# Optimization experiments

Hardware: AMD Instinct MI355X
Metric: run time of the kernel (lower is better)

## Reference

```python
import jax, jax.numpy as jnp
import numpy as np

NUM_HEADS = 16
EPS = 1e-12  # F.normalize default eps


def _l2norm(x):
    # F.normalize(x, dim=-1): x / max(||x||_2, eps)
    n = jnp.sqrt(jnp.sum(x * x, axis=-1, keepdims=True))
    return x / jnp.maximum(n, EPS)


def setup_inputs() -> dict:
    key = jax.random.key(0)
    k1, k2, k3 = jax.random.split(key, 3)
    B, N, C = 16, 3136, 768
    x = jax.random.normal(k1, (B, N, C), dtype=jnp.float32)
    qkv_w = jax.random.normal(k2, (C, 3 * C), dtype=jnp.float32) * (1.0 / np.sqrt(C))
    temperature = jnp.ones((NUM_HEADS, 1, 1), dtype=jnp.float32)
    proj_w = jax.random.normal(k3, (C, C), dtype=jnp.float32) * (1.0 / np.sqrt(C))
    proj_b = jnp.zeros((C,), dtype=jnp.float32)
    return {"x": x, "qkv_w": qkv_w, "temperature": temperature,
            "proj_w": proj_w, "proj_b": proj_b}


def reference(x, qkv_w, temperature, proj_w, proj_b):
    B, N, C = x.shape
    H = NUM_HEADS
    D = C // H
    # qkv: [B,N,3C] -> [B,N,3,H,D] -> (3,B,H,D,N)
    qkv = (x @ qkv_w).reshape(B, N, 3, H, D).transpose(2, 0, 3, 4, 1)
    q, k, v = qkv[0], qkv[1], qkv[2]  # each [B,H,D,N]
    qn = _l2norm(q)  # normalize over token axis N
    kn = _l2norm(k)
    # cross-covariance: [B,H,D,D]
    attn = jnp.einsum('bhdn,bhen->bhde', qn, kn) * temperature
    attn = jax.nn.softmax(attn, axis=-1)
    out = jnp.einsum('bhde,bhen->bhdn', attn, v)  # [B,H,D,N]
    out = out.transpose(0, 3, 1, 2).reshape(B, N, C)
    return out @ proj_w + proj_b
```

## Files before the change

### kernel.cpp

```cpp
#include <hip/hip_runtime.h>

typedef unsigned short u16;
typedef unsigned int   u32;
typedef __attribute__((ext_vector_type(4))) float f32x4;
typedef __attribute__((ext_vector_type(8))) short bf16x8;
typedef __attribute__((ext_vector_type(8))) unsigned short u16x8;

#define MFMA16(a,b,c) __builtin_amdgcn_mfma_f32_16x16x32_bf16(a,b,c,0,0,0)

#define PANEL 2408448u

__device__ __forceinline__ u16 f32_bf16(float f){
  u32 u = __builtin_bit_cast(u32, f);
  u = (u + 0x7FFFu + ((u >> 16) & 1u)) >> 16;
  return (u16)u;
}

__device__ __forceinline__ void async_cp16(const u16* g, u16* l){
  __builtin_amdgcn_global_load_lds((const __attribute__((address_space(1))) u32*)g,
                                   (__attribute__((address_space(3))) u32*)l, 16, 0, 0);
}

__global__ __launch_bounds__(256)
void cvt_f32_bf16(const float* __restrict__ in, u16* __restrict__ out){
  size_t i = ((size_t)blockIdx.x * 256 + threadIdx.x) * 8;
  f32x4 a = *(const f32x4*)(in + i);
  f32x4 b = *(const f32x4*)(in + i + 4);
  u16x8 o;
  o[0]=f32_bf16(a[0]); o[1]=f32_bf16(a[1]); o[2]=f32_bf16(a[2]); o[3]=f32_bf16(a[3]);
  o[4]=f32_bf16(b[0]); o[5]=f32_bf16(b[1]); o[6]=f32_bf16(b[2]); o[7]=f32_bf16(b[3]);
  *(u16x8*)(out + i) = o;
}

__global__ __launch_bounds__(256)
void transpose_cvt(const float* __restrict__ w, u16* __restrict__ wt, int K, int N){
  __shared__ float tile[32][33];
  int n0 = blockIdx.x * 32, k0 = blockIdx.y * 32;
  int tx = threadIdx.x, ty = threadIdx.y;
#pragma unroll
  for (int j = 0; j < 32; j += 8) tile[ty + j][tx] = w[(size_t)(k0 + ty + j) * N + n0 + tx];
  __syncthreads();
#pragma unroll
  for (int j = 0; j < 32; j += 8)
    wt[(size_t)(n0 + ty + j) * K + k0 + tx] = f32_bf16(tile[tx][ty + j]);
}

template<int OUT_BF16, int BIAS, int A_GATHER, int C_HEADS>
__global__ __launch_bounds__(256)
void gemm_bt(const u16* __restrict__ A, const u16* __restrict__ Bt,
             void* __restrict__ Cv, const float* __restrict__ bias,
             int K, int lda, int ldc){
  __shared__ u16 sA[128 * 64];
  __shared__ u16 sB[128 * 64];
  const int tid  = threadIdx.x;
  const int lane = tid & 63;
  const int wave = tid >> 6;
  const int lrow = lane & 15, quad = lane >> 4;
  const int m0 = blockIdx.y * 128, n0 = blockIdx.x * 128;
  const int wm = (wave & 1) * 64, wn = (wave >> 1) * 64;
  const int sw = lrow & 7;
  const int col0 = ((0 * 4 + quad) ^ sw) * 8;
  const int col1 = ((1 * 4 + quad) ^ sw) * 8;

  f32x4 acc[4][4];
#pragma unroll
  for (int i = 0; i < 4; i++)
#pragma unroll
    for (int j = 0; j < 4; j++) acc[i][j] = (f32x4){0.f, 0.f, 0.f, 0.f};

  for (int kt = 0; kt < K; kt += 64){
#pragma unroll
    for (int i = 0; i < 4; i++){
      int c = i * 256 + tid;
      int m = c >> 3, kc = (c & 7) ^ (m & 7);
      const u16* src;
      if (A_GATHER){
        unsigned k0 = (unsigned)(kt + kc * 8);
        unsigned hh = k0 / 48u;
        unsigned dd = k0 - hh * 48u;
        src = A + (size_t)hh * PANEL + (size_t)(m0 + m) * 48 + dd;
      } else {
        src = A + (size_t)(m0 + m) * lda + kt + kc * 8;
      }
      async_cp16(src, &sA[c * 8]);
    }
#pragma unroll
    for (int i = 0; i < 4; i++){
      int c = i * 256 + tid;
      int n = c >> 3, kc = (c & 7) ^ (n & 7);
      async_cp16(Bt + (size_t)(n0 + n) * K + kt + kc * 8, &sB[c * 8]);
    }
    __syncthreads();
#pragma unroll
    for (int kk = 0; kk < 2; kk++){
      const int col = kk ? col1 : col0;
      bf16x8 af[4], bfv[4];
#pragma unroll
      for (int mi = 0; mi < 4; mi++)
        af[mi] = *(const bf16x8*)&sA[(wm + mi * 16 + lrow) * 64 + col];
#pragma unroll
      for (int ni = 0; ni < 4; ni++)
        bfv[ni] = *(const bf16x8*)&sB[(wn + ni * 16 + lrow) * 64 + col];
#pragma unroll
      for (int mi = 0; mi < 4; mi++)
#pragma unroll
        for (int ni = 0; ni < 4; ni++)
          acc[mi][ni] = MFMA16(af[mi], bfv[ni], acc[mi][ni]);
    }
    __syncthreads();
  }
#pragma unroll
  for (int mi = 0; mi < 4; mi++){
#pragma unroll
    for (int ni = 0; ni < 4; ni++){
      int col = n0 + wn + ni * 16 + lrow;
      if (OUT_BF16 && C_HEADS){
        unsigned which = (unsigned)col / 768u;
        unsigned rem   = (unsigned)col - which * 768u;
        unsigned hh    = rem / 48u;
        unsigned dd    = rem - hh * 48u;
        u16* cb = (u16*)Cv + (size_t)(which * 16u + hh) * PANEL + dd;
#pragma unroll
        for (int r = 0; r < 4; r++){
          int row = m0 + wm + mi * 16 + quad * 4 + r;
          cb[(size_t)row * 48] = f32_bf16(acc[mi][ni][r]);
        }
      } else {
        float bv = BIAS ? bias[col] : 0.f;
#pragma unroll
        for (int r = 0; r < 4; r++){
          int row = m0 + wm + mi * 16 + quad * 4 + r;
          float v = acc[mi][ni][r];
          if (OUT_BF16) ((u16*)Cv)[(size_t)row * ldc + col] = f32_bf16(v);
          else          ((float*)Cv)[(size_t)row * ldc + col] = v + bv;
        }
      }
    }
  }
}

__global__ __launch_bounds__(256)
void attn_stats(const u16* __restrict__ qkv2, const float* __restrict__ temperature,
                u16* __restrict__ attnb){
  const int h = blockIdx.x, b = blockIdx.y;
  const int tid = threadIdx.x, wave = tid >> 6, lane = tid & 63;
  const int lrow = lane & 15, quad = lane >> 4;
  __shared__ struct {
    union {
      struct { u16 q[48 * 136]; u16 k[48 * 136]; } t;
      float red[2 * 15 * 256];
    } u;
    float S[48 * 49];
    float invq[48], invk[48];
  } sm;

  f32x4 acc[15];
#pragma unroll
  for (int t = 0; t < 15; t++) acc[t] = (f32x4){0.f, 0.f, 0.f, 0.f};

  const u16* qbase = qkv2 + (size_t)h        * PANEL + (size_t)b * 3136 * 48;
  const u16* kbase = qkv2 + (size_t)(16 + h) * PANEL + (size_t)b * 3136 * 48;

  for (int n0 = 0; n0 < 3136; n0 += 128){
    __syncthreads();
#pragma unroll
    for (int i = 0; i < 3; i++){
      int wgrp = i * 4 + wave;
      int qk = wgrp >= 6;
      int dg = qk ? wgrp - 6 : wgrp;
      int n  = n0 + lane * 2;
      const u16* src = (qk ? kbase : qbase) + (size_t)n * 48 + dg * 8;
      u16x8 va = (n     < 3136) ? *(const u16x8*)src        : (u16x8){0,0,0,0,0,0,0,0};
      u16x8 vb = (n + 1 < 3136) ? *(const u16x8*)(src + 48) : (u16x8){0,0,0,0,0,0,0,0};
      u16* dst = qk ? sm.u.t.k : sm.u.t.q;
#pragma unroll
      for (int j = 0; j < 8; j++)
        *(u32*)&dst[(dg * 8 + j) * 136 + lane * 2] = (u32)va[j] | ((u32)vb[j] << 16);
    }
    __syncthreads();
    bf16x8 qf[3], kf[3];
#pragma unroll
    for (int ti = 0; ti < 3; ti++){
      qf[ti] = *(const bf16x8*)&sm.u.t.q[(ti * 16 + lrow) * 136 + wave * 32 + quad * 8];
      kf[ti] = *(const bf16x8*)&sm.u.t.k[(ti * 16 + lrow) * 136 + wave * 32 + quad * 8];
    }
#pragma unroll
    for (int ti = 0; ti < 3; ti++)
#pragma unroll
      for (int tj = 0; tj < 3; tj++)
        acc[ti * 3 + tj] = MFMA16(qf[ti], kf[tj], acc[ti * 3 + tj]);
#pragma unroll
    for (int ti = 0; ti < 3; ti++){
      acc[9  + ti] = MFMA16(qf[ti], qf[ti], acc[9  + ti]);
      acc[12 + ti] = MFMA16(kf[ti], kf[ti], acc[12 + ti]);
    }
  }
  __syncthreads();
  if (wave < 2){
#pragma unroll
    for (int t = 0; t < 15; t++)
      *(f32x4*)&sm.u.red[(wave * 15 + t) * 256 + lane * 4] = acc[t];
  }
  __syncthreads();
  if (wave >= 2){
#pragma unroll
    for (int t = 0; t < 15; t++){
      f32x4* p = (f32x4*)&sm.u.red[((wave - 2) * 15 + t) * 256 + lane * 4];
      *p = *p + acc[t];
    }
  }
  __syncthreads();
  {
    const int p = tid;
    const int lr = p >> 2, rr = p & 3;
    const int row16 = ((lr >> 4) << 2) + rr, col16 = lr & 15;
#pragma unroll
    for (int t = 0; t < 9; t++){
      float v = sm.u.red[t * 256 + p] + sm.u.red[(15 + t) * 256 + p];
      sm.S[((t / 3) * 16 + row16) * 49 + (t % 3) * 16 + col16] = v;
    }
#pragma unroll
    for (int t = 9; t < 15; t++){
      float v = sm.u.red[t * 256 + p] + sm.u.red[(15 + t) * 256 + p];
      if (row16 == col16){
        if (t < 12) sm.invq[(t - 9)  * 16 + row16] = v;
        else        sm.invk[(t - 12) * 16 + row16] = v;
      }
    }
  }
  __syncthreads();
  if (tid < 96){
    float* arr = (tid < 48) ? sm.invq : sm.invk;
    int d = (tid < 48) ? tid : tid - 48;
    arr[d] = 1.0f / fmaxf(sqrtf(arr[d]), 1e-12f);
  }
  __syncthreads();
  if (tid < 48){
    const int d = tid;
    const float scale = sm.invq[d] * temperature[h];
    float lg[48];
    float mx = -1e30f;
#pragma unroll
    for (int e = 0; e < 48; e++){
      lg[e] = sm.S[d * 49 + e] * scale * sm.invk[e];
      mx = fmaxf(mx, lg[e]);
    }
    float s = 0.f;
#pragma unroll
    for (int e = 0; e < 48; e++){ float ex = __expf(lg[e] - mx); lg[e] = ex; s += ex; }
    const float inv = 1.f / s;
    u16* dst = attnb + ((size_t)(b * 16 + h) * 48 + d) * 64;
#pragma unroll
    for (int e = 0; e < 48; e++) dst[e] = f32_bf16(lg[e] * inv);
#pragma unroll
    for (int e = 48; e < 64; e++) dst[e] = 0;
  }
}

__global__ __launch_bounds__(256)
void attn_apply_v(const u16* __restrict__ qkv2, const u16* __restrict__ attnb,
                  u16* __restrict__ outm){
  const int h = blockIdx.y, b = blockIdx.z;
  const int nb = blockIdx.x * 256;
  const int tid = threadIdx.x, wave = tid >> 6, lane = tid & 63;
  const int lrow = lane & 15, quad = lane >> 4;
  __shared__ u16 sA[48 * 72];
#pragma unroll
  for (int i = 0; i < 2; i++){
    int idx = i * 256 + tid;
    if (idx < 384){
      int d = idx >> 3, eg = idx & 7;
      *(u16x8*)&sA[d * 72 + eg * 8] =
        *(const u16x8*)&attnb[((size_t)(b * 16 + h) * 48 + d) * 64 + eg * 8];
    }
  }
  __syncthreads();
  bf16x8 bfr[3][2];
#pragma unroll
  for (int tj = 0; tj < 3; tj++){
    bfr[tj][0] = *(const bf16x8*)&sA[(tj * 16 + lrow) * 72 + quad * 8];
    bfr[tj][1] = *(const bf16x8*)&sA[(tj * 16 + lrow) * 72 + 32 + quad * 8];
  }
  f32x4 acc[4][3];
#pragma unroll
  for (int i = 0; i < 4; i++)
#pragma unroll
    for (int j = 0; j < 3; j++) acc[i][j] = (f32x4){0.f, 0.f, 0.f, 0.f};

  const u16* vpanel = qkv2 + (size_t)(32 + h) * PANEL + (size_t)b * 3136 * 48;
  const int eo1 = 32 + ((quad < 2) ? quad * 8 : 0);
#pragma unroll
  for (int mi = 0; mi < 4; mi++){
    int n = nb + wave * 64 + mi * 16 + lrow;
    int nc = n < 3136 ? n : 3135;
    const u16* vp = vpanel + (size_t)nc * 48;
    bf16x8 a0 = *(const bf16x8*)(vp + quad * 8);
    bf16x8 a1 = *(const bf16x8*)(vp + eo1);
#pragma unroll
    for (int tj = 0; tj < 3; tj++){
      acc[mi][tj] = MFMA16(a0, bfr[tj][0], acc[mi][tj]);
      acc[mi][tj] = MFMA16(a1, bfr[tj][1], acc[mi][tj]);
    }
  }
  u16* opanel = outm + (size_t)h * PANEL + (size_t)b * 3136 * 48;
#pragma unroll
  for (int mi = 0; mi < 4; mi++)
#pragma unroll
    for (int tj = 0; tj < 3; tj++){
      int d = tj * 16 + lrow;
#pragma unroll
      for (int r = 0; r < 4; r++){
        int n = nb + wave * 64 + mi * 16 + quad * 4 + r;
        if (n < 3136) opanel[(size_t)n * 48 + d] = f32_bf16(acc[mi][tj][r]);
      }
    }
}

extern "C" void kernel_launch(void* const* d_in, const int* in_sizes, int n_in,
                              void* d_out, int out_size, void* d_ws, size_t ws_size,
                              hipStream_t stream){
  const float* x      = (const float*)d_in[0];
  const float* qkv_w  = (const float*)d_in[1];
  const float* temp   = (const float*)d_in[2];
  const float* proj_w = (const float*)d_in[3];
  const float* proj_b = (const float*)d_in[4];
  float* out = (float*)d_out;
  char* ws = (char*)d_ws;

  const size_t OFF_XB   = 0;
  const size_t OFF_WQ   = 77070336;
  const size_t OFF_WP   = 80609280;
  const size_t OFF_QKV  = 81788928;
  const size_t OFF_ATTN = 312999936;

  u16* xb    = (u16*)(ws + OFF_XB);
  u16* wqt   = (u16*)(ws + OFF_WQ);
  u16* wpt   = (u16*)(ws + OFF_WP);
  u16* qkv2  = (u16*)(ws + OFF_QKV);
  u16* attnb = (u16*)(ws + OFF_ATTN);

  cvt_f32_bf16<<<dim3(18816), dim3(256), 0, stream>>>(x, xb);
  transpose_cvt<<<dim3(2304 / 32, 768 / 32), dim3(32, 8), 0, stream>>>(qkv_w, wqt, 768, 2304);
  transpose_cvt<<<dim3(768 / 32, 768 / 32), dim3(32, 8), 0, stream>>>(proj_w, wpt, 768, 768);
  gemm_bt<1, 0, 0, 1><<<dim3(18, 392), dim3(256), 0, stream>>>(xb, wqt, qkv2, nullptr, 768, 768, 0);
  attn_stats<<<dim3(16, 16), dim3(256), 0, stream>>>(qkv2, temp, attnb);
  attn_apply_v<<<dim3(13, 16, 16), dim3(256), 0, stream>>>(qkv2, attnb, qkv2);
  gemm_bt<0, 1, 1, 0><<<dim3(6, 392), dim3(256), 0, stream>>>(qkv2, wpt, out, proj_b, 768, 0, 768);
}
```

Before: 687.0 us.

## Replace GEMM with 256x256 double-buffered pipelined kernel and XCD-aware block remap

```diff
diff --git a/kernel.cpp b/kernel.cpp
--- a/kernel.cpp
+++ b/kernel.cpp
@@ -45,75 +45,140 @@
     wt[(size_t)(n0 + ty + j) * K + k0 + tx] = f32_bf16(tile[tx][ty + j]);
 }
 
+template<int A_GATHER>
+__device__ __forceinline__ void stage_half(const u16* __restrict__ G, u16* __restrict__ lds,
+                                           int tid, int row0, int base, int kt, int ld){
+#pragma unroll
+  for (int i = 0; i < 2; i++){
+    int c = i * 512 + tid;
+    int r = c >> 3;
+    int kc = (c & 7) ^ (r & 7);
+    const u16* src;
+    if (A_GATHER){
+      unsigned k0 = (unsigned)(kt + kc * 8);
+      unsigned hh = k0 / 48u, dd = k0 - hh * 48u;
+      src = G + (size_t)hh * PANEL + (size_t)(base + row0 + r) * 48 + dd;
+    } else {
+      src = G + (size_t)(base + row0 + r) * ld + kt + kc * 8;
+    }
+    async_cp16(src, lds + ((size_t)(row0 + r) * 64 + (c & 7) * 8));
+  }
+}
+
 template<int OUT_BF16, int BIAS, int A_GATHER, int C_HEADS>
-__global__ __launch_bounds__(256)
-void gemm_bt(const u16* __restrict__ A, const u16* __restrict__ Bt,
+__global__ __launch_bounds__(512, 2)
+void gemm256(const u16* __restrict__ A, const u16* __restrict__ Bt,
              void* __restrict__ Cv, const float* __restrict__ bias,
-             int K, int lda, int ldc){
-  __shared__ u16 sA[128 * 64];
-  __shared__ u16 sB[128 * 64];
+             int K, int lda, int ldc, int nbx){
+  __shared__ u16 sA[2][256 * 64];
+  __shared__ u16 sB[2][256 * 64];
   const int tid  = threadIdx.x;
-  const int lane = tid & 63;
-  const int wave = tid >> 6;
+  const int lane = tid & 63, wave = tid >> 6;
   const int lrow = lane & 15, quad = lane >> 4;
-  const int m0 = blockIdx.y * 128, n0 = blockIdx.x * 128;
-  const int wm = (wave & 1) * 64, wn = (wave >> 1) * 64;
+  const int wr = wave >> 2, wc = wave & 3;
+
+  const int nwg = (int)gridDim.x;
+  const int bid = (int)blockIdx.x;
+  const int qq = nwg >> 3, rm = nwg & 7;
+  const int xcd = bid & 7, jj = bid >> 3;
+  const int f = (xcd < rm ? xcd * (qq + 1) : rm * (qq + 1) + (xcd - rm) * qq) + jj;
+  const int bx = f % nbx, by = f / nbx;
+  const int m0 = by * 256, n0 = bx * 256;
+
   const int sw = lrow & 7;
-  const int col0 = ((0 * 4 + quad) ^ sw) * 8;
-  const int col1 = ((1 * 4 + quad) ^ sw) * 8;
-
-  f32x4 acc[4][4];
-#pragma unroll
-  for (int i = 0; i < 4; i++)
+  const int colK0 = (quad ^ sw) * 8;
+  const int colK1 = ((4 + quad) ^ sw) * 8;
+
+  f32x4 acc[8][4];
+#pragma unroll
+  for (int i = 0; i < 8; i++)
 #pragma unroll
     for (int j = 0; j < 4; j++) acc[i][j] = (f32x4){0.f, 0.f, 0.f, 0.f};
 
-  for (int kt = 0; kt < K; kt += 64){
-#pragma unroll
-    for (int i = 0; i < 4; i++){
-      int c = i * 256 + tid;
-      int m = c >> 3, kc = (c & 7) ^ (m & 7);
-      const u16* src;
-      if (A_GATHER){
-        unsigned k0 = (unsigned)(kt + kc * 8);
-        unsigned hh = k0 / 48u;
-        unsigned dd = k0 - hh * 48u;
-        src = A + (size_t)hh * PANEL + (size_t)(m0 + m) * 48 + dd;
-      } else {
-        src = A + (size_t)(m0 + m) * lda + kt + kc * 8;
-      }
-      async_cp16(src, &sA[c * 8]);
-    }
-#pragma unroll
-    for (int i = 0; i < 4; i++){
-      int c = i * 256 + tid;
-      int n = c >> 3, kc = (c & 7) ^ (n & 7);
-      async_cp16(Bt + (size_t)(n0 + n) * K + kt + kc * 8, &sB[c * 8]);
-    }
-    __syncthreads();
-#pragma unroll
-    for (int kk = 0; kk < 2; kk++){
-      const int col = kk ? col1 : col0;
-      bf16x8 af[4], bfv[4];
-#pragma unroll
-      for (int mi = 0; mi < 4; mi++)
-        af[mi] = *(const bf16x8*)&sA[(wm + mi * 16 + lrow) * 64 + col];
-#pragma unroll
-      for (int ni = 0; ni < 4; ni++)
-        bfv[ni] = *(const bf16x8*)&sB[(wn + ni * 16 + lrow) * 64 + col];
-#pragma unroll
-      for (int mi = 0; mi < 4; mi++)
-#pragma unroll
-        for (int ni = 0; ni < 4; ni++)
-          acc[mi][ni] = MFMA16(af[mi], bfv[ni], acc[mi][ni]);
-    }
-    __syncthreads();
-  }
-#pragma unroll
-  for (int mi = 0; mi < 4; mi++){
+  const int nt = K >> 6;
+  stage_half<A_GATHER>(A, sA[0], tid, 0,   m0, 0, lda);
+  stage_half<A_GATHER>(A, sA[0], tid, 128, m0, 0, lda);
+  stage_half<0>(Bt, sB[0], tid, 0,   n0, 0, K);
+  stage_half<0>(Bt, sB[0], tid, 128, n0, 0, K);
+  stage_half<A_GATHER>(A, sA[1], tid, 0,   m0, 64, lda);
+  stage_half<A_GATHER>(A, sA[1], tid, 128, m0, 64, lda);
+  asm volatile("s_waitcnt vmcnt(4)" ::: "memory");
+  __builtin_amdgcn_s_barrier();
+
+#pragma unroll 1
+  for (int t = 0; t < nt; ++t){
+    u16* sAb = sA[t & 1];
+    u16* sBb = sB[t & 1];
+    u16* sBn = sB[(t & 1) ^ 1];
+    const int kt1 = (t + 1) << 6, kt2 = (t + 2) << 6;
+    bf16x8 A0[8], A1[8], B0[4], B1[4];
+
+#pragma unroll
+    for (int mi = 0; mi < 8; mi++)
+      A0[mi] = *(const bf16x8*)&sAb[(wr * 128 + mi * 16 + lrow) * 64 + colK0];
+#pragma unroll
+    for (int ni = 0; ni < 4; ni++)
+      B0[ni] = *(const bf16x8*)&sBb[(wc * 64 + ni * 16 + lrow) * 64 + colK0];
+    if (t + 1 < nt) stage_half<0>(Bt, sBn, tid, 0, n0, kt1, K);
+    __builtin_amdgcn_s_barrier();
+    asm volatile("s_waitcnt lgkmcnt(0)" ::: "memory");
+    __builtin_amdgcn_s_setprio(1);
+#pragma unroll
+    for (int mi = 0; mi < 8; mi++){
+      acc[mi][0] = MFMA16(A0[mi], B0[0], acc[mi][0]);
+      acc[mi][1] = MFMA16(A0[mi], B0[1], acc[mi][1]);
+    }
+    __builtin_amdgcn_s_setprio(0);
+    __builtin_amdgcn_s_barrier();
+
+#pragma unroll
+    for (int mi = 0; mi < 8; mi++)
+      A1[mi] = *(const bf16x8*)&sAb[(wr * 128 + mi * 16 + lrow) * 64 + colK1];
+#pragma unroll
+    for (int ni = 0; ni < 4; ni++)
+      B1[ni] = *(const bf16x8*)&sBb[(wc * 64 + ni * 16 + lrow) * 64 + colK1];
+    if (t + 1 < nt) stage_half<0>(Bt, sBn, tid, 128, n0, kt1, K);
+    __builtin_amdgcn_s_barrier();
+    asm volatile("s_waitcnt lgkmcnt(0)" ::: "memory");
+    __builtin_amdgcn_s_setprio(1);
+#pragma unroll
+    for (int mi = 0; mi < 8; mi++){
+      acc[mi][2] = MFMA16(A0[mi], B0[2], acc[mi][2]);
+      acc[mi][3] = MFMA16(A0[mi], B0[3], acc[mi][3]);
+    }
+    __builtin_amdgcn_s_setprio(0);
+    __builtin_amdgcn_s_barrier();
+
+    if (t + 2 < nt) stage_half<A_GATHER>(A, sAb, tid, 0, m0, kt2, lda);
+    __builtin_amdgcn_s_barrier();
+    __builtin_amdgcn_s_setprio(1);
+#pragma unroll
+    for (int mi = 0; mi < 8; mi++){
+      acc[mi][0] = MFMA16(A1[mi], B1[0], acc[mi][0]);
+      acc[mi][1] = MFMA16(A1[mi], B1[1], acc[mi][1]);
+    }
+    __builtin_amdgcn_s_setprio(0);
+    __builtin_amdgcn_s_barrier();
+
+    if (t + 2 < nt) stage_half<A_GATHER>(A, sAb, tid, 128, m0, kt2, lda);
+    __builtin_amdgcn_s_barrier();
+    __builtin_amdgcn_s_setprio(1);
+#pragma unroll
+    for (int mi = 0; mi < 8; mi++){
+      acc[mi][2] = MFMA16(A1[mi], B1[2], acc[mi][2]);
+      acc[mi][3] = MFMA16(A1[mi], B1[3], acc[mi][3]);
+    }
+    __builtin_amdgcn_s_setprio(0);
+    if (t + 2 < nt)      asm volatile("s_waitcnt vmcnt(4)" ::: "memory");
+    else if (t + 1 < nt) asm volatile("s_waitcnt vmcnt(0)" ::: "memory");
+    __builtin_amdgcn_s_barrier();
+  }
+
+#pragma unroll
+  for (int mi = 0; mi < 8; mi++){
 #pragma unroll
     for (int ni = 0; ni < 4; ni++){
-      int col = n0 + wn + ni * 16 + lrow;
+      const int col = n0 + wc * 64 + ni * 16 + lrow;
       if (OUT_BF16 && C_HEADS){
         unsigned which = (unsigned)col / 768u;
         unsigned rem   = (unsigned)col - which * 768u;
@@ -122,14 +187,14 @@
         u16* cb = (u16*)Cv + (size_t)(which * 16u + hh) * PANEL + dd;
 #pragma unroll
         for (int r = 0; r < 4; r++){
-          int row = m0 + wm + mi * 16 + quad * 4 + r;
+          int row = m0 + wr * 128 + mi * 16 + quad * 4 + r;
           cb[(size_t)row * 48] = f32_bf16(acc[mi][ni][r]);
         }
       } else {
         float bv = BIAS ? bias[col] : 0.f;
 #pragma unroll
         for (int r = 0; r < 4; r++){
-          int row = m0 + wm + mi * 16 + quad * 4 + r;
+          int row = m0 + wr * 128 + mi * 16 + quad * 4 + r;
           float v = acc[mi][ni][r];
           if (OUT_BF16) ((u16*)Cv)[(size_t)row * ldc + col] = f32_bf16(v);
           else          ((float*)Cv)[(size_t)row * ldc + col] = v + bv;
@@ -212,8 +277,8 @@
   __syncthreads();
   {
     const int p = tid;
-    const int lr = p >> 2, rr = p & 3;
-    const int row16 = ((lr >> 4) << 2) + rr, col16 = lr & 15;
+    const int lr = p >> 2, r = p & 3;
+    const int row16 = ((lr >> 4) << 2) + r, col16 = lr & 15;
 #pragma unroll
     for (int t = 0; t < 9; t++){
       float v = sm.u.red[t * 256 + p] + sm.u.red[(15 + t) * 256 + p];
@@ -342,8 +407,8 @@
   cvt_f32_bf16<<<dim3(18816), dim3(256), 0, stream>>>(x, xb);
   transpose_cvt<<<dim3(2304 / 32, 768 / 32), dim3(32, 8), 0, stream>>>(qkv_w, wqt, 768, 2304);
   transpose_cvt<<<dim3(768 / 32, 768 / 32), dim3(32, 8), 0, stream>>>(proj_w, wpt, 768, 768);
-  gemm_bt<1, 0, 0, 1><<<dim3(18, 392), dim3(256), 0, stream>>>(xb, wqt, qkv2, nullptr, 768, 768, 0);
+  gemm256<1, 0, 0, 1><<<dim3(1764), dim3(512), 0, stream>>>(xb, wqt, qkv2, nullptr, 768, 768, 0, 9);
   attn_stats<<<dim3(16, 16), dim3(256), 0, stream>>>(qkv2, temp, attnb);
   attn_apply_v<<<dim3(13, 16, 16), dim3(256), 0, stream>>>(qkv2, attnb, qkv2);
-  gemm_bt<0, 1, 1, 0><<<dim3(6, 392), dim3(256), 0, stream>>>(qkv2, wpt, out, proj_b, 768, 0, 768);
-}
+  gemm256<0, 1, 1, 0><<<dim3(588), dim3(512), 0, stream>>>(qkv2, wpt, out, proj_b, 768, 0, 768, 3);
+}
```

After: 664.3 us. 1.03x faster.
